# Kernel tuning notes

Hardware: AMD Instinct MI355X
Metric: run time of the kernel (lower is better)

Reference implementation:

```python
import jax, jax.numpy as jnp
import numpy as np

N = 100000  # number of nodes (batch of Irreps objects)
MUL = {'0e': 128, '1o': 64, '2e': 32}  # multiplicities per irrep id
DIM = {'0e': 1, '1o': 3, '2e': 5}      # 2l+1 per irrep id


def setup_inputs() -> dict:
    key = jax.random.key(0)
    ks = jax.random.split(key, 7)
    x0e = jax.random.normal(ks[0], (N, MUL['0e'], DIM['0e']), dtype=jnp.float32)
    x1o = jax.random.normal(ks[1], (N, MUL['1o'], DIM['1o']), dtype=jnp.float32)
    x2e = jax.random.normal(ks[2], (N, MUL['2e'], DIM['2e']), dtype=jnp.float32)
    # one (2l+1)-vector of weights per (output copy, input copy), grouped per irrep id
    w0e = jax.random.normal(ks[3], (MUL['0e'], MUL['0e'], DIM['0e']), dtype=jnp.float32)
    w1o = jax.random.normal(ks[4], (MUL['1o'], MUL['1o'], DIM['1o']), dtype=jnp.float32)
    w2e = jax.random.normal(ks[5], (MUL['2e'], MUL['2e'], DIM['2e']), dtype=jnp.float32)
    bias = jax.random.normal(ks[6], (MUL['0e'],), dtype=jnp.float32)  # one bias per 0e output
    return {"x0e": x0e, "x1o": x1o, "x2e": x2e, "w0e": w0e, "w1o": w1o, "w2e": w2e, "bias": bias}


def reference(x0e, x1o, x2e, w0e, w1o, w2e, bias):
    # Per irrep id: out[n, o, m] = sum_i x[n, i, m] * w[o, i, m]  (elementwise over m)
    y0e = jnp.einsum('nim,oim->nom', x0e, w0e) + bias[None, :, None]
    y1o = jnp.einsum('nim,oim->nom', x1o, w1o)
    y2e = jnp.einsum('nim,oim->nom', x2e, w2e)
    n = x0e.shape[0]
    # Flatten irreps back into a single feature vector per node (sorted id order: 0e, 1o, 2e)
    return jnp.concatenate([y0e.reshape(n, -1), y1o.reshape(n, -1), y2e.reshape(n, -1)], axis=-1)
```

## Files before the change

kernel.cpp:

```cpp
#include <hip/hip_runtime.h>


#define OUT_STRIDE 480

__global__ __launch_bounds__(256) void lin0e_kernel(
    const float* __restrict__ x, const float* __restrict__ w,
    const float* __restrict__ bias, float* __restrict__ out, int n_nodes) {
  __shared__ float wT[128 * 129];
  for (int f = threadIdx.x; f < 128 * 128; f += 256) {
    int o = f >> 7, k = f & 127;
    wT[k * 129 + o] = w[f];
  }
  __syncthreads();

  const int o = threadIdx.x & 127;
  const int half = threadIdx.x >> 7;
  const int n0 = (blockIdx.x * 2 + half) * 16;
  if (n0 >= n_nodes) return;
  const float bv = bias[o];
  const float* __restrict__ xb = x + (size_t)n0 * 128;
  float* __restrict__ ob = out + (size_t)n0 * OUT_STRIDE + o;

  if (n0 + 16 <= n_nodes) {
    float acc[16];
#pragma unroll
    for (int t = 0; t < 16; ++t) acc[t] = 0.f;
#pragma unroll 4
    for (int k = 0; k < 128; ++k) {
      float wv = wT[k * 129 + o];
#pragma unroll
      for (int t = 0; t < 16; ++t)
        acc[t] = fmaf(xb[t * 128 + k], wv, acc[t]);
    }
#pragma unroll
    for (int t = 0; t < 16; ++t) ob[(size_t)t * OUT_STRIDE] = acc[t] + bv;
  } else {
    for (int t = 0; t < n_nodes - n0; ++t) {
      float acc = 0.f;
      for (int k = 0; k < 128; ++k)
        acc = fmaf(xb[t * 128 + k], wT[k * 129 + o], acc);
      ob[(size_t)t * OUT_STRIDE] = acc + bv;
    }
  }
}

__global__ __launch_bounds__(256) void lin1o_kernel(
    const float* __restrict__ x, const float* __restrict__ w,
    float* __restrict__ out, int n_nodes) {
  __shared__ float wT[192 * 65];
  for (int f = threadIdx.x; f < 64 * 192; f += 256) {
    int o = f / 192, j = f - o * 192;
    wT[j * 65 + o] = w[f];
  }
  __syncthreads();

  const int o = threadIdx.x & 63;
  const int wv_ = threadIdx.x >> 6;
  const int n0 = (blockIdx.x * 4 + wv_) * 8;
  if (n0 >= n_nodes) return;
  const float* __restrict__ xb = x + (size_t)n0 * 192;
  float* __restrict__ ob = out + (size_t)n0 * OUT_STRIDE + 128 + o * 3;

  if (n0 + 8 <= n_nodes) {
    float a0[8], a1[8], a2[8];
#pragma unroll
    for (int t = 0; t < 8; ++t) { a0[t] = 0.f; a1[t] = 0.f; a2[t] = 0.f; }
#pragma unroll 2
    for (int k = 0; k < 64; ++k) {
      float w0 = wT[(k * 3 + 0) * 65 + o];
      float w1 = wT[(k * 3 + 1) * 65 + o];
      float w2 = wT[(k * 3 + 2) * 65 + o];
#pragma unroll
      for (int t = 0; t < 8; ++t) {
        a0[t] = fmaf(xb[t * 192 + k * 3 + 0], w0, a0[t]);
        a1[t] = fmaf(xb[t * 192 + k * 3 + 1], w1, a1[t]);
        a2[t] = fmaf(xb[t * 192 + k * 3 + 2], w2, a2[t]);
      }
    }
#pragma unroll
    for (int t = 0; t < 8; ++t) {
      ob[(size_t)t * OUT_STRIDE + 0] = a0[t];
      ob[(size_t)t * OUT_STRIDE + 1] = a1[t];
      ob[(size_t)t * OUT_STRIDE + 2] = a2[t];
    }
  } else {
    for (int t = 0; t < n_nodes - n0; ++t) {
      float a0 = 0.f, a1 = 0.f, a2 = 0.f;
      for (int k = 0; k < 64; ++k) {
        a0 = fmaf(xb[t * 192 + k * 3 + 0], wT[(k * 3 + 0) * 65 + o], a0);
        a1 = fmaf(xb[t * 192 + k * 3 + 1], wT[(k * 3 + 1) * 65 + o], a1);
        a2 = fmaf(xb[t * 192 + k * 3 + 2], wT[(k * 3 + 2) * 65 + o], a2);
      }
      ob[(size_t)t * OUT_STRIDE + 0] = a0;
      ob[(size_t)t * OUT_STRIDE + 1] = a1;
      ob[(size_t)t * OUT_STRIDE + 2] = a2;
    }
  }
}

__global__ __launch_bounds__(256) void lin2e_kernel(
    const float* __restrict__ x, const float* __restrict__ w,
    float* __restrict__ out, int n_nodes) {
  __shared__ float wT[160 * 33];
  for (int f = threadIdx.x; f < 32 * 160; f += 256) {
    int o = f / 160, j = f - o * 160;
    wT[j * 33 + o] = w[f];
  }
  __syncthreads();

  const int o = threadIdx.x & 31;
  const bool store_lane = ((threadIdx.x >> 5) & 1) == 0;
  const int wv_ = threadIdx.x >> 6;
  const int n0 = (blockIdx.x * 4 + wv_) * 8;
  if (n0 >= n_nodes) return;
  const float* __restrict__ xb = x + (size_t)n0 * 160;
  float* __restrict__ ob = out + (size_t)n0 * OUT_STRIDE + 320 + o * 5;

  if (n0 + 8 <= n_nodes) {
    float a[5][8];
#pragma unroll
    for (int m = 0; m < 5; ++m)
#pragma unroll
      for (int t = 0; t < 8; ++t) a[m][t] = 0.f;
    for (int k = 0; k < 32; ++k) {
      float wm[5];
#pragma unroll
      for (int m = 0; m < 5; ++m) wm[m] = wT[(k * 5 + m) * 33 + o];
#pragma unroll
      for (int t = 0; t < 8; ++t) {
#pragma unroll
        for (int m = 0; m < 5; ++m)
          a[m][t] = fmaf(xb[t * 160 + k * 5 + m], wm[m], a[m][t]);
      }
    }
    if (store_lane) {
#pragma unroll
      for (int t = 0; t < 8; ++t) {
#pragma unroll
        for (int m = 0; m < 5; ++m)
          ob[(size_t)t * OUT_STRIDE + m] = a[m][t];
      }
    }
  } else {
    if (store_lane) {
      for (int t = 0; t < n_nodes - n0; ++t) {
        for (int m = 0; m < 5; ++m) {
          float acc = 0.f;
          for (int k = 0; k < 32; ++k)
            acc = fmaf(xb[t * 160 + k * 5 + m], wT[(k * 5 + m) * 33 + o], acc);
          ob[(size_t)t * OUT_STRIDE + m] = acc;
        }
      }
    }
  }
}

extern "C" void kernel_launch(void* const* d_in, const int* in_sizes, int n_in,
                              void* d_out, int out_size, void* d_ws, size_t ws_size,
                              hipStream_t stream) {
  const float* x0e = (const float*)d_in[0];
  const float* x1o = (const float*)d_in[1];
  const float* x2e = (const float*)d_in[2];
  const float* w0e = (const float*)d_in[3];
  const float* w1o = (const float*)d_in[4];
  const float* w2e = (const float*)d_in[5];
  const float* bias = (const float*)d_in[6];
  float* out = (float*)d_out;

  const int n = in_sizes[0] / 128;

  const int b0 = (n + 31) / 32;
  const int b12 = (n + 31) / 32;

  lin0e_kernel<<<b0, 256, 0, stream>>>(x0e, w0e, bias, out, n);
  lin1o_kernel<<<b12, 256, 0, stream>>>(x1o, w1o, out, n);
  lin2e_kernel<<<b12, 256, 0, stream>>>(x2e, w2e, out, n);
}
```

Before: 858.6 us.

## Replace per-irrep kernels with templated shared-memory tiled GEMM with double buffering

Replaces the three hand-written kernels with one templated kernel. It stages node and weight chunks in LDS, splits them into per-m planes with padded rows, and register-tiles outputs over several nodes and output channels. The next chunk is loaded into registers while the current one is computed, using double-buffered shared memory. This targets the old kernels' redundant global reads of x per thread and scalar FMAs, at the cost of more registers, LDS scatter transposes, and strided output stores.

```diff
diff --git a/kernel.cpp b/kernel.cpp
--- a/kernel.cpp
+++ b/kernel.cpp
@@ -1,154 +1,179 @@
 #include <hip/hip_runtime.h>
 
-
 #define OUT_STRIDE 480
 
-__global__ __launch_bounds__(256) void lin0e_kernel(
+__device__ __forceinline__ float dot4acc(float4 a, float4 b, float acc) {
+  acc = fmaf(a.x, b.x, acc);
+  acc = fmaf(a.y, b.y, acc);
+  acc = fmaf(a.z, b.z, acc);
+  acc = fmaf(a.w, b.w, acc);
+  return acc;
+}
+
+template<int MUL, int M, int OBLK, int WAVES_O, int TO, int TT, int IC, int OUT_OFF, bool HAS_BIAS>
+__global__ __launch_bounds__(256, 2) void lin_kernel(
     const float* __restrict__ x, const float* __restrict__ w,
-    const float* __restrict__ bias, float* __restrict__ out, int n_nodes) {
-  __shared__ float wT[128 * 129];
-  for (int f = threadIdx.x; f < 128 * 128; f += 256) {
-    int o = f >> 7, k = f & 127;
-    wT[k * 129 + o] = w[f];
+    const float* __restrict__ bias, float* __restrict__ out, int n_nodes)
+{
+  constexpr int K = MUL;
+  constexpr int R = K * M;
+  constexpr int CF = IC * M;
+  constexpr int C4 = CF / 4;
+  constexpr int RS = (IC % 8 == 4) ? IC : IC + 4;
+  constexpr int WAVES_T = 4 / WAVES_O;
+  constexpr int TROW = 8 * TT;
+  constexpr int TTILE = WAVES_T * TROW;
+  constexpr int CHUNKS = K / IC;
+  constexpr int XPLANE = TTILE * RS;
+  constexpr int XSZ = M * XPLANE;
+  constexpr int WPLANE = OBLK * RS;
+  constexpr int WSZ = M * WPLANE;
+  constexpr int NX4 = TTILE * CF / 4;
+  constexpr int NW4 = OBLK * CF / 4;
+  constexpr int XLD = (NX4 + 255) / 256;
+  constexpr int WLD = (NW4 + 255) / 256;
+
+  __shared__ float xs[2 * XSZ];
+  __shared__ float ws[2 * WSZ];
+
+  const int tid = threadIdx.x;
+  const int lane = tid & 63;
+  const int wv = tid >> 6;
+  const int lane_o = lane & 7;
+  const int lane_t = lane >> 3;
+  const int wo = (WAVES_O > 1) ? (wv % WAVES_O) : 0;
+  const int tr = wv / WAVES_O;
+
+  const int blk_t0 = blockIdx.x * TTILE;
+  const int o_grid = blockIdx.y * OBLK;
+
+  float4 xr[XLD];
+  float4 wr[WLD];
+
+  auto load_chunk = [&](int c) {
+#pragma unroll
+    for (int l = 0; l < XLD; ++l) {
+      int idx = tid + l * 256;
+      if (XLD * 256 == NX4 || idx < NX4) {
+        int t = idx / C4, q = idx - t * C4;
+        int gt = blk_t0 + t;
+        if (gt < n_nodes)
+          xr[l] = *(const float4*)(x + (size_t)gt * R + c * CF + q * 4);
+        else
+          xr[l] = make_float4(0.f, 0.f, 0.f, 0.f);
+      }
+    }
+#pragma unroll
+    for (int l = 0; l < WLD; ++l) {
+      int idx = tid + l * 256;
+      if (WLD * 256 == NW4 || idx < NW4) {
+        int o = idx / C4, q = idx - o * C4;
+        wr[l] = *(const float4*)(w + (size_t)(o_grid + o) * R + c * CF + q * 4);
+      }
+    }
+  };
+
+  auto write_chunk = [&](int buf) {
+    float* xb = xs + buf * XSZ;
+    float* wb = ws + buf * WSZ;
+#pragma unroll
+    for (int l = 0; l < XLD; ++l) {
+      int idx = tid + l * 256;
+      if (XLD * 256 == NX4 || idx < NX4) {
+        int t = idx / C4, q = idx - t * C4;
+        if (M == 1) {
+          *(float4*)(xb + t * RS + q * 4) = xr[l];
+        } else {
+          float v[4] = {xr[l].x, xr[l].y, xr[l].z, xr[l].w};
+#pragma unroll
+          for (int e = 0; e < 4; ++e) {
+            int off = q * 4 + e;
+            int i = off / M, m = off - i * M;
+            xb[m * XPLANE + t * RS + i] = v[e];
+          }
+        }
+      }
+    }
+#pragma unroll
+    for (int l = 0; l < WLD; ++l) {
+      int idx = tid + l * 256;
+      if (WLD * 256 == NW4 || idx < NW4) {
+        int o = idx / C4, q = idx - o * C4;
+        if (M == 1) {
+          *(float4*)(wb + o * RS + q * 4) = wr[l];
+        } else {
+          float v[4] = {wr[l].x, wr[l].y, wr[l].z, wr[l].w};
+#pragma unroll
+          for (int e = 0; e < 4; ++e) {
+            int off = q * 4 + e;
+            int i = off / M, m = off - i * M;
+            wb[m * WPLANE + o * RS + i] = v[e];
+          }
+        }
+      }
+    }
+  };
+
+  float acc[M][TO][TT];
+#pragma unroll
+  for (int m = 0; m < M; ++m)
+#pragma unroll
+    for (int jo = 0; jo < TO; ++jo)
+#pragma unroll
+      for (int j = 0; j < TT; ++j) acc[m][jo][j] = 0.f;
+
+  load_chunk(0);
+  write_chunk(0);
+  __syncthreads();
+
+  for (int c = 0; c < CHUNKS; ++c) {
+    if (c + 1 < CHUNKS) load_chunk(c + 1);
+    const int buf = c & 1;
+    const float* xbase = xs + buf * XSZ + (tr * TROW) * RS;
+    const float* wbase = ws + buf * WSZ + (wo * 8 * TO) * RS;
+#pragma unroll
+    for (int i4 = 0; i4 < IC / 4; ++i4) {
+#pragma unroll
+      for (int m = 0; m < M; ++m) {
+        const float* xp = xbase + m * XPLANE + i4 * 4;
+        const float* wp = wbase + m * WPLANE + i4 * 4;
+        float4 xf[TT];
+#pragma unroll
+        for (int j = 0; j < TT; ++j)
+          xf[j] = *(const float4*)(xp + (j * 8 + lane_t) * RS);
+        float4 wf[TO];
+#pragma unroll
+        for (int jo = 0; jo < TO; ++jo)
+          wf[jo] = *(const float4*)(wp + (jo * 8 + lane_o) * RS);
+#pragma unroll
+        for (int jo = 0; jo < TO; ++jo)
+#pragma unroll
+          for (int j = 0; j < TT; ++j)
+            acc[m][jo][j] = dot4acc(xf[j], wf[jo], acc[m][jo][j]);
+      }
+    }
+    if (c + 1 < CHUNKS) write_chunk((c + 1) & 1);
+    __syncthreads();
   }
-  __syncthreads();
-
-  const int o = threadIdx.x & 127;
-  const int half = threadIdx.x >> 7;
-  const int n0 = (blockIdx.x * 2 + half) * 16;
-  if (n0 >= n_nodes) return;
-  const float bv = bias[o];
-  const float* __restrict__ xb = x + (size_t)n0 * 128;
-  float* __restrict__ ob = out + (size_t)n0 * OUT_STRIDE + o;
-
-  if (n0 + 16 <= n_nodes) {
-    float acc[16];
-#pragma unroll
-    for (int t = 0; t < 16; ++t) acc[t] = 0.f;
-#pragma unroll 4
-    for (int k = 0; k < 128; ++k) {
-      float wv = wT[k * 129 + o];
-#pragma unroll
-      for (int t = 0; t < 16; ++t)
-        acc[t] = fmaf(xb[t * 128 + k], wv, acc[t]);
-    }
-#pragma unroll
-    for (int t = 0; t < 16; ++t) ob[(size_t)t * OUT_STRIDE] = acc[t] + bv;
-  } else {
-    for (int t = 0; t < n_nodes - n0; ++t) {
-      float acc = 0.f;
-      for (int k = 0; k < 128; ++k)
-        acc = fmaf(xb[t * 128 + k], wT[k * 129 + o], acc);
-      ob[(size_t)t * OUT_STRIDE] = acc + bv;
-    }
+
+  float bv[TO];
+  if (HAS_BIAS) {
+#pragma unroll
+    for (int jo = 0; jo < TO; ++jo)
+      bv[jo] = bias[o_grid + wo * 8 * TO + jo * 8 + lane_o];
   }
-}
-
-__global__ __launch_bounds__(256) void lin1o_kernel(
-    const float* __restrict__ x, const float* __restrict__ w,
-    float* __restrict__ out, int n_nodes) {
-  __shared__ float wT[192 * 65];
-  for (int f = threadIdx.x; f < 64 * 192; f += 256) {
-    int o = f / 192, j = f - o * 192;
-    wT[j * 65 + o] = w[f];
-  }
-  __syncthreads();
-
-  const int o = threadIdx.x & 63;
-  const int wv_ = threadIdx.x >> 6;
-  const int n0 = (blockIdx.x * 4 + wv_) * 8;
-  if (n0 >= n_nodes) return;
-  const float* __restrict__ xb = x + (size_t)n0 * 192;
-  float* __restrict__ ob = out + (size_t)n0 * OUT_STRIDE + 128 + o * 3;
-
-  if (n0 + 8 <= n_nodes) {
-    float a0[8], a1[8], a2[8];
-#pragma unroll
-    for (int t = 0; t < 8; ++t) { a0[t] = 0.f; a1[t] = 0.f; a2[t] = 0.f; }
-#pragma unroll 2
-    for (int k = 0; k < 64; ++k) {
-      float w0 = wT[(k * 3 + 0) * 65 + o];
-      float w1 = wT[(k * 3 + 1) * 65 + o];
-      float w2 = wT[(k * 3 + 2) * 65 + o];
-#pragma unroll
-      for (int t = 0; t < 8; ++t) {
-        a0[t] = fmaf(xb[t * 192 + k * 3 + 0], w0, a0[t]);
-        a1[t] = fmaf(xb[t * 192 + k * 3 + 1], w1, a1[t]);
-        a2[t] = fmaf(xb[t * 192 + k * 3 + 2], w2, a2[t]);
-      }
-    }
-#pragma unroll
-    for (int t = 0; t < 8; ++t) {
-      ob[(size_t)t * OUT_STRIDE + 0] = a0[t];
-      ob[(size_t)t * OUT_STRIDE + 1] = a1[t];
-      ob[(size_t)t * OUT_STRIDE + 2] = a2[t];
-    }
-  } else {
-    for (int t = 0; t < n_nodes - n0; ++t) {
-      float a0 = 0.f, a1 = 0.f, a2 = 0.f;
-      for (int k = 0; k < 64; ++k) {
-        a0 = fmaf(xb[t * 192 + k * 3 + 0], wT[(k * 3 + 0) * 65 + o], a0);
-        a1 = fmaf(xb[t * 192 + k * 3 + 1], wT[(k * 3 + 1) * 65 + o], a1);
-        a2 = fmaf(xb[t * 192 + k * 3 + 2], wT[(k * 3 + 2) * 65 + o], a2);
-      }
-      ob[(size_t)t * OUT_STRIDE + 0] = a0;
-      ob[(size_t)t * OUT_STRIDE + 1] = a1;
-      ob[(size_t)t * OUT_STRIDE + 2] = a2;
-    }
-  }
-}
-
-__global__ __launch_bounds__(256) void lin2e_kernel(
-    const float* __restrict__ x, const float* __restrict__ w,
-    float* __restrict__ out, int n_nodes) {
-  __shared__ float wT[160 * 33];
-  for (int f = threadIdx.x; f < 32 * 160; f += 256) {
-    int o = f / 160, j = f - o * 160;
-    wT[j * 33 + o] = w[f];
-  }
-  __syncthreads();
-
-  const int o = threadIdx.x & 31;
-  const bool store_lane = ((threadIdx.x >> 5) & 1) == 0;
-  const int wv_ = threadIdx.x >> 6;
-  const int n0 = (blockIdx.x * 4 + wv_) * 8;
-  if (n0 >= n_nodes) return;
-  const float* __restrict__ xb = x + (size_t)n0 * 160;
-  float* __restrict__ ob = out + (size_t)n0 * OUT_STRIDE + 320 + o * 5;
-
-  if (n0 + 8 <= n_nodes) {
-    float a[5][8];
-#pragma unroll
-    for (int m = 0; m < 5; ++m)
-#pragma unroll
-      for (int t = 0; t < 8; ++t) a[m][t] = 0.f;
-    for (int k = 0; k < 32; ++k) {
-      float wm[5];
-#pragma unroll
-      for (int m = 0; m < 5; ++m) wm[m] = wT[(k * 5 + m) * 33 + o];
-#pragma unroll
-      for (int t = 0; t < 8; ++t) {
-#pragma unroll
-        for (int m = 0; m < 5; ++m)
-          a[m][t] = fmaf(xb[t * 160 + k * 5 + m], wm[m], a[m][t]);
-      }
-    }
-    if (store_lane) {
-#pragma unroll
-      for (int t = 0; t < 8; ++t) {
-#pragma unroll
-        for (int m = 0; m < 5; ++m)
-          ob[(size_t)t * OUT_STRIDE + m] = a[m][t];
-      }
-    }
-  } else {
-    if (store_lane) {
-      for (int t = 0; t < n_nodes - n0; ++t) {
-        for (int m = 0; m < 5; ++m) {
-          float acc = 0.f;
-          for (int k = 0; k < 32; ++k)
-            acc = fmaf(xb[t * 160 + k * 5 + m], wT[(k * 5 + m) * 33 + o], acc);
-          ob[(size_t)t * OUT_STRIDE + m] = acc;
+#pragma unroll
+  for (int j = 0; j < TT; ++j) {
+    int t = blk_t0 + tr * TROW + j * 8 + lane_t;
+    if (t < n_nodes) {
+#pragma unroll
+      for (int jo = 0; jo < TO; ++jo) {
+        int o = o_grid + wo * 8 * TO + jo * 8 + lane_o;
+#pragma unroll
+        for (int m = 0; m < M; ++m) {
+          float v = acc[m][jo][j];
+          if (HAS_BIAS) v += bv[jo];
+          out[(size_t)t * OUT_STRIDE + OUT_OFF + o * M + m] = v;
         }
       }
     }
@@ -169,10 +194,16 @@
 
   const int n = in_sizes[0] / 128;
 
-  const int b0 = (n + 31) / 32;
-  const int b12 = (n + 31) / 32;
-
-  lin0e_kernel<<<b0, 256, 0, stream>>>(x0e, w0e, bias, out, n);
-  lin1o_kernel<<<b12, 256, 0, stream>>>(x1o, w1o, out, n);
-  lin2e_kernel<<<b12, 256, 0, stream>>>(x2e, w2e, out, n);
+  dim3 blk(256);
+
+  dim3 g0((n + 255) / 256, 2);
+  lin_kernel<128, 1, 64, 1, 8, 8, 16, 0, true>
+      <<<g0, blk, 0, stream>>>(x0e, w0e, bias, out, n);
+
+  dim3 g1((n + 127) / 128, 1);
+  lin_kernel<64, 3, 64, 2, 4, 8, 8, 128, false>
+      <<<g1, blk, 0, stream>>>(x1o, w1o, nullptr, out, n);
+
+  lin_kernel<32, 5, 32, 1, 4, 4, 4, 320, false>
+      <<<g1, blk, 0, stream>>>(x2e, w2e, nullptr, out, n);
 }
```

Measured after the change: 1.306 ms. +52.1%, slower.
